# Kernel optimization log

Hardware: AMD Instinct MI355X
Metric: run time of the kernel (lower is better)

The kernel has to match this reference:

```python
import jax, jax.numpy as jnp
import numpy as np

D_IN, D_OUT, RANK, N = 4096, 4096, 16, 8192


def _quantize_weight(w, bits):
    # round-to-nearest fake quantization, stored back as floats (as in the torch code)
    absmax = jnp.abs(w).max()
    scale = (2 ** (bits - 1) - 1) / absmax
    q = jnp.clip(jnp.round(w * scale), -2 ** (bits - 1), 2 ** (bits - 1) - 1)
    return q / scale


def _double_quantization(w, bits):
    absmax = jnp.abs(w).max()
    c1 = (2 ** (bits - 1) - 1) / absmax          # scalar fp32 scale
    q = jnp.clip(jnp.round(w * c1), -2 ** (bits - 1), 2 ** (bits - 1) - 1)
    return c1, q / c1                             # c_kbit_2 has same shape as w


def setup_inputs() -> dict:
    key = jax.random.key(0)
    kX, kW, kL1, kL2 = jax.random.split(key, 4)
    X = jax.random.normal(kX, (N, D_IN), dtype=jnp.float32)
    W0 = jax.random.normal(kW, (D_IN, D_OUT), dtype=jnp.float32)
    W_nf4 = _quantize_weight(W0, bits=4)
    c_fp32_1, c_kbit_2 = _double_quantization(W_nf4, bits=8)
    L1 = jax.random.normal(kL1, (D_IN, RANK), dtype=jnp.float32)
    L2 = jax.random.normal(kL2, (RANK, D_OUT), dtype=jnp.float32)
    return {"X": X, "W_nf4": W_nf4, "c_fp32_1": c_fp32_1,
            "c_kbit_2": c_kbit_2, "L1": L1, "L2": L2}


def reference(X, W_nf4, c_fp32_1, c_kbit_2, L1, L2):
    # dequantize: elementwise scalar * elementwise-tensor scaling of stored weight
    W = W_nf4 * c_fp32_1 * c_kbit_2               # [D_IN, D_OUT]
    # main GEMM + low-rank LoRA path, added in the epilogue
    Y = X @ W + (X @ L1) @ L2                     # [N, D_OUT]
    return Y
```

## Files before the change

### kernel.cpp

```cpp
#include <hip/hip_runtime.h>


#define M_ROWS 8192
#define K_DIM  4096
#define N_OUT  4096
#define CVT_BLOCKS 16384
#define WP_BLOCKS  8192
#define TR_BLOCKS  32

typedef float  f32x16 __attribute__((ext_vector_type(16)));
typedef __bf16 bf16x8 __attribute__((ext_vector_type(8)));
typedef float  f32x4  __attribute__((ext_vector_type(4)));
typedef unsigned short ushort8v __attribute__((ext_vector_type(8)));

__device__ float          Tg[(size_t)M_ROWS * 16];
__device__ unsigned short L1t[16 * K_DIM];
__device__ unsigned short L2t[N_OUT * 16];

__device__ __forceinline__ unsigned short f2bf(float f) {
    __bf16 h = (__bf16)f;
    union { __bf16 h; unsigned short u; } v; v.h = h;
    return v.u;
}

__global__ __launch_bounds__(256) void prep_kernel(
        const float* __restrict__ X,    ushort8v* __restrict__ Xh,
        const float* __restrict__ Wnf4, const float* __restrict__ c1p,
        const float* __restrict__ c2,   const float* __restrict__ L1,
        const float* __restrict__ L2,   unsigned short* __restrict__ Wt) {
    const int t = threadIdx.x;

    if (blockIdx.x < CVT_BLOCKS) {
        size_t tid = (size_t)blockIdx.x * 256 + t;
        const float4* xp = (const float4*)X;
        float4 a = xp[tid * 2];
        float4 b = xp[tid * 2 + 1];
        ushort8v o;
        o[0] = f2bf(a.x); o[1] = f2bf(a.y); o[2] = f2bf(a.z); o[3] = f2bf(a.w);
        o[4] = f2bf(b.x); o[5] = f2bf(b.y); o[6] = f2bf(b.z); o[7] = f2bf(b.w);
        Xh[tid] = o;
        return;
    }

    if (blockIdx.x < CVT_BLOCKS + WP_BLOCKS) {
        const int wb = blockIdx.x - CVT_BLOCKS;
        const int n  = (wb & 63) * 64 + (t & 63);
        const int k0 = (wb >> 6) * 32 + (t >> 6) * 8;
        const float c1 = *c1p;
        ushort8v o;
        #pragma unroll
        for (int kk = 0; kk < 8; ++kk) {
            size_t g = (size_t)(k0 + kk) * N_OUT + n;
            o[kk] = f2bf(Wnf4[g] * c1 * c2[g]);
        }
        *(ushort8v*)&Wt[(size_t)n * K_DIM + k0] = o;
        return;
    }

    const int idx = (blockIdx.x - CVT_BLOCKS - WP_BLOCKS) * 256 + t;
    if (idx < K_DIM) {
        const float4* lp = (const float4*)&L1[(size_t)idx * 16];
        float4 r0 = lp[0], r1 = lp[1], r2 = lp[2], r3 = lp[3];
        float v[16] = {r0.x, r0.y, r0.z, r0.w, r1.x, r1.y, r1.z, r1.w,
                       r2.x, r2.y, r2.z, r2.w, r3.x, r3.y, r3.z, r3.w};
        #pragma unroll
        for (int r = 0; r < 16; ++r)
            L1t[(size_t)r * K_DIM + idx] = f2bf(v[r]);
    } else {
        const int n = idx - K_DIM;
        ushort8v a, b;
        #pragma unroll
        for (int r = 0; r < 8; ++r) a[r] = f2bf(L2[(size_t)r * N_OUT + n]);
        #pragma unroll
        for (int r = 0; r < 8; ++r) b[r] = f2bf(L2[(size_t)(r + 8) * N_OUT + n]);
        *(ushort8v*)&L2t[(size_t)n * 16]     = a;
        *(ushort8v*)&L2t[(size_t)n * 16 + 8] = b;
    }
}

__global__ __launch_bounds__(64) void xl1_kernel(const __bf16* __restrict__ Xh) {
    const int m0   = blockIdx.x * 16;
    const int lane = threadIdx.x;
    const int l15  = lane & 15;
    const int l4   = lane >> 4;

    const __bf16* ap = Xh + (size_t)(m0 + l15) * K_DIM + l4 * 8;
    const __bf16* bp = (const __bf16*)L1t + (size_t)l15 * K_DIM + l4 * 8;

    f32x4 acc = {};
    #pragma unroll 8
    for (int k = 0; k < K_DIM; k += 32) {
        bf16x8 af = *(const bf16x8*)(ap + k);
        bf16x8 bf = *(const bf16x8*)(bp + k);
        acc = __builtin_amdgcn_mfma_f32_16x16x32_bf16(af, bf, acc, 0, 0, 0);
    }
    #pragma unroll
    for (int reg = 0; reg < 4; ++reg)
        Tg[(size_t)(m0 + l4 * 4 + reg) * 16 + l15] = acc[reg];
}

__global__ __launch_bounds__(256) void gemm_bt_kernel(
        const __bf16* __restrict__ A, const __bf16* __restrict__ Bt,
        float* __restrict__ C) {
    __shared__ __bf16 As[128 * 32];
    __shared__ __bf16 Bs[128 * 32];

    const int t    = threadIdx.x;
    const int w    = t >> 6;
    const int lane = t & 63;
    const int half = lane >> 5;
    const int l32  = lane & 31;
    const int m0   = blockIdx.y * 128;
    const int n0   = blockIdx.x * 128;
    const int wm   = (w >> 1) * 64;
    const int wn   = (w & 1) * 64;

    const int srow = lane >> 2;
    const int scol = ((lane & 3) ^ ((lane >> 3) & 3)) * 8;
    const int rsw = (l32 >> 1) & 3;

    f32x16 acc[2][2] = {};

    for (int kb = 0; kb < K_DIM; kb += 32) {
        __syncthreads();
        #pragma unroll
        for (int j = 0; j < 2; ++j) {
            int row = w * 32 + j * 16 + srow;
            const __bf16* gp = A + (size_t)(m0 + row) * K_DIM + kb + scol;
            __builtin_amdgcn_global_load_lds(
                (const __attribute__((address_space(1))) unsigned int*)gp,
                (__attribute__((address_space(3))) unsigned int*)(As + (w * 32 + j * 16) * 32),
                16, 0, 0);
        }
        #pragma unroll
        for (int j = 0; j < 2; ++j) {
            int row = w * 32 + j * 16 + srow;
            const __bf16* gp = Bt + (size_t)(n0 + row) * K_DIM + kb + scol;
            __builtin_amdgcn_global_load_lds(
                (const __attribute__((address_space(1))) unsigned int*)gp,
                (__attribute__((address_space(3))) unsigned int*)(Bs + (w * 32 + j * 16) * 32),
                16, 0, 0);
        }
        __syncthreads();

        bf16x8 af[2][2], bf[2][2];
        #pragma unroll
        for (int mt = 0; mt < 2; ++mt)
            #pragma unroll
            for (int ks = 0; ks < 2; ++ks) {
                int row = wm + mt * 32 + l32;
                int slot = (2 * ks + half) ^ rsw;
                af[mt][ks] = *(const bf16x8*)(As + row * 32 + slot * 8);
            }
        #pragma unroll
        for (int nt = 0; nt < 2; ++nt)
            #pragma unroll
            for (int ks = 0; ks < 2; ++ks) {
                int row = wn + nt * 32 + l32;
                int slot = (2 * ks + half) ^ rsw;
                bf[nt][ks] = *(const bf16x8*)(Bs + row * 32 + slot * 8);
            }

        #pragma unroll
        for (int ks = 0; ks < 2; ++ks)
            #pragma unroll
            for (int mt = 0; mt < 2; ++mt)
                #pragma unroll
                for (int nt = 0; nt < 2; ++nt)
                    acc[mt][nt] = __builtin_amdgcn_mfma_f32_32x32x16_bf16(
                        af[mt][ks], bf[nt][ks], acc[mt][nt], 0, 0, 0);
    }

    {
        bf16x8 afl[2], bfl[2];
        #pragma unroll
        for (int mt = 0; mt < 2; ++mt) {
            const float* tp = Tg + (size_t)(m0 + wm + mt * 32 + l32) * 16 + half * 8;
            float4 p0 = *(const float4*)tp;
            float4 p1 = *(const float4*)(tp + 4);
            afl[mt][0] = (__bf16)p0.x; afl[mt][1] = (__bf16)p0.y;
            afl[mt][2] = (__bf16)p0.z; afl[mt][3] = (__bf16)p0.w;
            afl[mt][4] = (__bf16)p1.x; afl[mt][5] = (__bf16)p1.y;
            afl[mt][6] = (__bf16)p1.z; afl[mt][7] = (__bf16)p1.w;
        }
        #pragma unroll
        for (int nt = 0; nt < 2; ++nt)
            bfl[nt] = *(const bf16x8*)((const __bf16*)L2t +
                        (size_t)(n0 + wn + nt * 32 + l32) * 16 + half * 8);
        #pragma unroll
        for (int mt = 0; mt < 2; ++mt)
            #pragma unroll
            for (int nt = 0; nt < 2; ++nt)
                acc[mt][nt] = __builtin_amdgcn_mfma_f32_32x32x16_bf16(
                    afl[mt], bfl[nt], acc[mt][nt], 0, 0, 0);
    }

    #pragma unroll
    for (int mt = 0; mt < 2; ++mt)
        #pragma unroll
        for (int nt = 0; nt < 2; ++nt) {
            int col = n0 + wn + nt * 32 + l32;
            #pragma unroll
            for (int reg = 0; reg < 16; ++reg) {
                int row = m0 + wm + mt * 32 + (reg & 3) + 8 * (reg >> 2) + 4 * half;
                C[(size_t)row * N_OUT + col] = acc[mt][nt][reg];
            }
        }
}

extern "C" void kernel_launch(void* const* d_in, const int* in_sizes, int n_in,
                              void* d_out, int out_size, void* d_ws, size_t ws_size,
                              hipStream_t stream) {
    const float* X    = (const float*)d_in[0];
    const float* Wnf4 = (const float*)d_in[1];
    const float* c1   = (const float*)d_in[2];
    const float* c2   = (const float*)d_in[3];
    const float* L1   = (const float*)d_in[4];
    const float* L2   = (const float*)d_in[5];
    float* Y = (float*)d_out;

    unsigned short* Xh = (unsigned short*)d_ws;
    unsigned short* Wt = (unsigned short*)((char*)d_ws + (size_t)M_ROWS * K_DIM * 2);

    prep_kernel<<<CVT_BLOCKS + WP_BLOCKS + TR_BLOCKS, 256, 0, stream>>>(
        X, (ushort8v*)Xh, Wnf4, c1, c2, L1, L2, Wt);
    xl1_kernel<<<M_ROWS / 16, 64, 0, stream>>>((const __bf16*)Xh);
    gemm_bt_kernel<<<dim3(N_OUT / 128, M_ROWS / 128), 256, 0, stream>>>(
        (const __bf16*)Xh, (const __bf16*)Wt, Y);
}
```

Before: 649.3 us.

## Split prep kernels, LDS-transpose weights, split-K xl1, swizzle and deepen GEMM K-step

Splits the fused prep kernel into separate conversion, weight-prep and LoRA-prep kernels. Weight prep now reads coalesced float4 rows and transposes them through an LDS tile before writing bf16. The X@L1 kernel spreads K across four waves and reduces the partial sums in shared memory to get more parallelism. The main GEMM remaps block indices so neighbouring blocks share tiles in L2, and it loads two 32-wide K slabs per barrier pair to halve synchronisation. The trade-offs are more kernel launches and twice the LDS per GEMM block.

Result: slower. 663.0 us (+2.1%).

```diff
diff --git a/kernel.cpp b/kernel.cpp
--- a/kernel.cpp
+++ b/kernel.cpp
@@ -5,12 +5,11 @@
 #define K_DIM  4096
 #define N_OUT  4096
 #define CVT_BLOCKS 16384
-#define WP_BLOCKS  8192
-#define TR_BLOCKS  32
+#define WP_BLOCKS  4096
 
 typedef float  f32x16 __attribute__((ext_vector_type(16)));
+typedef float  f32x4  __attribute__((ext_vector_type(4)));
 typedef __bf16 bf16x8 __attribute__((ext_vector_type(8)));
-typedef float  f32x4  __attribute__((ext_vector_type(4)));
 typedef unsigned short ushort8v __attribute__((ext_vector_type(8)));
 
 __device__ float          Tg[(size_t)M_ROWS * 16];
@@ -23,41 +22,54 @@
     return v.u;
 }
 
-__global__ __launch_bounds__(256) void prep_kernel(
-        const float* __restrict__ X,    ushort8v* __restrict__ Xh,
+__global__ __launch_bounds__(256) void cvt_kernel(
+        const float* __restrict__ X, ushort8v* __restrict__ Xh) {
+    size_t tid = (size_t)blockIdx.x * 256 + threadIdx.x;
+    const float4* xp = (const float4*)X;
+    float4 a = xp[tid * 2];
+    float4 b = xp[tid * 2 + 1];
+    ushort8v o;
+    o[0] = f2bf(a.x); o[1] = f2bf(a.y); o[2] = f2bf(a.z); o[3] = f2bf(a.w);
+    o[4] = f2bf(b.x); o[5] = f2bf(b.y); o[6] = f2bf(b.z); o[7] = f2bf(b.w);
+    Xh[tid] = o;
+}
+
+__global__ __launch_bounds__(256) void wprep_kernel(
         const float* __restrict__ Wnf4, const float* __restrict__ c1p,
-        const float* __restrict__ c2,   const float* __restrict__ L1,
-        const float* __restrict__ L2,   unsigned short* __restrict__ Wt) {
-    const int t = threadIdx.x;
-
-    if (blockIdx.x < CVT_BLOCKS) {
-        size_t tid = (size_t)blockIdx.x * 256 + t;
-        const float4* xp = (const float4*)X;
-        float4 a = xp[tid * 2];
-        float4 b = xp[tid * 2 + 1];
-        ushort8v o;
-        o[0] = f2bf(a.x); o[1] = f2bf(a.y); o[2] = f2bf(a.z); o[3] = f2bf(a.w);
-        o[4] = f2bf(b.x); o[5] = f2bf(b.y); o[6] = f2bf(b.z); o[7] = f2bf(b.w);
-        Xh[tid] = o;
-        return;
-    }
-
-    if (blockIdx.x < CVT_BLOCKS + WP_BLOCKS) {
-        const int wb = blockIdx.x - CVT_BLOCKS;
-        const int n  = (wb & 63) * 64 + (t & 63);
-        const int k0 = (wb >> 6) * 32 + (t >> 6) * 8;
-        const float c1 = *c1p;
-        ushort8v o;
-        #pragma unroll
-        for (int kk = 0; kk < 8; ++kk) {
-            size_t g = (size_t)(k0 + kk) * N_OUT + n;
-            o[kk] = f2bf(Wnf4[g] * c1 * c2[g]);
-        }
-        *(ushort8v*)&Wt[(size_t)n * K_DIM + k0] = o;
-        return;
-    }
-
-    const int idx = (blockIdx.x - CVT_BLOCKS - WP_BLOCKS) * 256 + t;
+        const float* __restrict__ c2,   unsigned short* __restrict__ Wt) {
+    __shared__ unsigned short tile[64][72];
+    const int t  = threadIdx.x;
+    const int wb = blockIdx.x;
+    const int n0 = (wb & 63) * 64;
+    const int k0 = (wb >> 6) * 64;
+    const float c1 = *c1p;
+
+    #pragma unroll
+    for (int i = 0; i < 4; ++i) {
+        int idx = i * 1024 + t * 4;
+        int k = idx >> 6, n4 = idx & 63;
+        size_t g = (size_t)(k0 + k) * N_OUT + n0 + n4;
+        float4 w = *(const float4*)&Wnf4[g];
+        float4 s = *(const float4*)&c2[g];
+        tile[n4    ][k] = f2bf(w.x * c1 * s.x);
+        tile[n4 + 1][k] = f2bf(w.y * c1 * s.y);
+        tile[n4 + 2][k] = f2bf(w.z * c1 * s.z);
+        tile[n4 + 3][k] = f2bf(w.w * c1 * s.w);
+    }
+    __syncthreads();
+
+    #pragma unroll
+    for (int i = 0; i < 2; ++i) {
+        int task = i * 256 + t;
+        int n = task >> 3, k8 = (task & 7) * 8;
+        ushort8v o = *(const ushort8v*)&tile[n][k8];
+        *(ushort8v*)&Wt[(size_t)(n0 + n) * K_DIM + k0 + k8] = o;
+    }
+}
+
+__global__ __launch_bounds__(256) void lorap_kernel(
+        const float* __restrict__ L1, const float* __restrict__ L2) {
+    const int idx = blockIdx.x * 256 + threadIdx.x;
     if (idx < K_DIM) {
         const float4* lp = (const float4*)&L1[(size_t)idx * 16];
         float4 r0 = lp[0], r1 = lp[1], r2 = lp[2], r3 = lp[3];
@@ -78,40 +90,71 @@
     }
 }
 
-__global__ __launch_bounds__(64) void xl1_kernel(const __bf16* __restrict__ Xh) {
-    const int m0   = blockIdx.x * 16;
-    const int lane = threadIdx.x;
-    const int l15  = lane & 15;
-    const int l4   = lane >> 4;
-
-    const __bf16* ap = Xh + (size_t)(m0 + l15) * K_DIM + l4 * 8;
-    const __bf16* bp = (const __bf16*)L1t + (size_t)l15 * K_DIM + l4 * 8;
-
+__global__ __launch_bounds__(256) void xl1_kernel(const __bf16* __restrict__ Xh) {
+    __shared__ float red[4][256];
+    const int m0 = blockIdx.x * 16;
+    const int t = threadIdx.x, wv = t >> 6, lane = t & 63;
+    const int l15 = lane & 15, l4 = lane >> 4;
+    const __bf16* ap = Xh + (size_t)(m0 + l15) * K_DIM + wv * 1024 + l4 * 8;
+    const __bf16* bp = (const __bf16*)L1t + (size_t)l15 * K_DIM + wv * 1024 + l4 * 8;
     f32x4 acc = {};
     #pragma unroll 8
-    for (int k = 0; k < K_DIM; k += 32) {
-        bf16x8 af = *(const bf16x8*)(ap + k);
-        bf16x8 bf = *(const bf16x8*)(bp + k);
-        acc = __builtin_amdgcn_mfma_f32_16x16x32_bf16(af, bf, acc, 0, 0, 0);
-    }
-    #pragma unroll
-    for (int reg = 0; reg < 4; ++reg)
-        Tg[(size_t)(m0 + l4 * 4 + reg) * 16 + l15] = acc[reg];
-}
+    for (int k = 0; k < 1024; k += 32) {
+        bf16x8 a = *(const bf16x8*)(ap + k);
+        bf16x8 b = *(const bf16x8*)(bp + k);
+        acc = __builtin_amdgcn_mfma_f32_16x16x32_bf16(a, b, acc, 0, 0, 0);
+    }
+    #pragma unroll
+    for (int r = 0; r < 4; ++r) red[wv][(l4 * 4 + r) * 16 + l15] = acc[r];
+    __syncthreads();
+    if (wv == 0) {
+        #pragma unroll
+        for (int r = 0; r < 4; ++r) {
+            int e = (l4 * 4 + r) * 16 + l15;
+            Tg[(size_t)(m0 + l4 * 4 + r) * 16 + l15] =
+                red[0][e] + red[1][e] + red[2][e] + red[3][e];
+        }
+    }
+}
+
+#define COMPUTE(B) do { \
+    bf16x8 af[2][2], bf[2][2]; \
+    _Pragma("unroll") for (int mt = 0; mt < 2; ++mt) \
+      _Pragma("unroll") for (int ks = 0; ks < 2; ++ks) { \
+        int row = wm + mt * 32 + l32; \
+        int slot = (2 * ks + half) ^ rsw; \
+        af[mt][ks] = *(const bf16x8*)(&As[B][0] + row * 32 + slot * 8); \
+      } \
+    _Pragma("unroll") for (int nt = 0; nt < 2; ++nt) \
+      _Pragma("unroll") for (int ks = 0; ks < 2; ++ks) { \
+        int row = wn + nt * 32 + l32; \
+        int slot = (2 * ks + half) ^ rsw; \
+        bf[nt][ks] = *(const bf16x8*)(&Bs[B][0] + row * 32 + slot * 8); \
+      } \
+    _Pragma("unroll") for (int ks = 0; ks < 2; ++ks) \
+      _Pragma("unroll") for (int mt = 0; mt < 2; ++mt) \
+        _Pragma("unroll") for (int nt = 0; nt < 2; ++nt) \
+          acc[mt][nt] = __builtin_amdgcn_mfma_f32_32x32x16_bf16( \
+              af[mt][ks], bf[nt][ks], acc[mt][nt], 0, 0, 0); \
+} while (0)
 
 __global__ __launch_bounds__(256) void gemm_bt_kernel(
         const __bf16* __restrict__ A, const __bf16* __restrict__ Bt,
         float* __restrict__ C) {
-    __shared__ __bf16 As[128 * 32];
-    __shared__ __bf16 Bs[128 * 32];
+    __shared__ __bf16 As[2][128 * 32];
+    __shared__ __bf16 Bs[2][128 * 32];
 
     const int t    = threadIdx.x;
     const int w    = t >> 6;
     const int lane = t & 63;
     const int half = lane >> 5;
     const int l32  = lane & 31;
-    const int m0   = blockIdx.y * 128;
-    const int n0   = blockIdx.x * 128;
+
+    const int bid = blockIdx.x;
+    const int swz = (bid & 7) * 256 + (bid >> 3);
+    const int m0  = (swz >> 5) * 128;
+    const int n0  = (swz & 31) * 128;
+
     const int wm   = (w >> 1) * 64;
     const int wn   = (w & 1) * 64;
 
@@ -121,54 +164,35 @@
 
     f32x16 acc[2][2] = {};
 
-    for (int kb = 0; kb < K_DIM; kb += 32) {
+    for (int kb = 0; kb < K_DIM; kb += 64) {
         __syncthreads();
         #pragma unroll
-        for (int j = 0; j < 2; ++j) {
-            int row = w * 32 + j * 16 + srow;
-            const __bf16* gp = A + (size_t)(m0 + row) * K_DIM + kb + scol;
-            __builtin_amdgcn_global_load_lds(
-                (const __attribute__((address_space(1))) unsigned int*)gp,
-                (__attribute__((address_space(3))) unsigned int*)(As + (w * 32 + j * 16) * 32),
-                16, 0, 0);
-        }
-        #pragma unroll
-        for (int j = 0; j < 2; ++j) {
-            int row = w * 32 + j * 16 + srow;
-            const __bf16* gp = Bt + (size_t)(n0 + row) * K_DIM + kb + scol;
-            __builtin_amdgcn_global_load_lds(
-                (const __attribute__((address_space(1))) unsigned int*)gp,
-                (__attribute__((address_space(3))) unsigned int*)(Bs + (w * 32 + j * 16) * 32),
-                16, 0, 0);
+        for (int b = 0; b < 2; ++b) {
+            #pragma unroll
+            for (int j = 0; j < 2; ++j) {
+                int row = w * 32 + j * 16 + srow;
+                const __bf16* gp = A + (size_t)(m0 + row) * K_DIM + kb + b * 32 + scol;
+                __builtin_amdgcn_global_load_lds(
+                    (const __attribute__((address_space(1))) unsigned int*)gp,
+                    (__attribute__((address_space(3))) unsigned int*)
+                        (&As[b][0] + (w * 32 + j * 16) * 32),
+                    16, 0, 0);
+            }
+            #pragma unroll
+            for (int j = 0; j < 2; ++j) {
+                int row = w * 32 + j * 16 + srow;
+                const __bf16* gp = Bt + (size_t)(n0 + row) * K_DIM + kb + b * 32 + scol;
+                __builtin_amdgcn_global_load_lds(
+                    (const __attribute__((address_space(1))) unsigned int*)gp,
+                    (__attribute__((address_space(3))) unsigned int*)
+                        (&Bs[b][0] + (w * 32 + j * 16) * 32),
+                    16, 0, 0);
+            }
         }
         __syncthreads();
 
-        bf16x8 af[2][2], bf[2][2];
-        #pragma unroll
-        for (int mt = 0; mt < 2; ++mt)
-            #pragma unroll
-            for (int ks = 0; ks < 2; ++ks) {
-                int row = wm + mt * 32 + l32;
-                int slot = (2 * ks + half) ^ rsw;
-                af[mt][ks] = *(const bf16x8*)(As + row * 32 + slot * 8);
-            }
-        #pragma unroll
-        for (int nt = 0; nt < 2; ++nt)
-            #pragma unroll
-            for (int ks = 0; ks < 2; ++ks) {
-                int row = wn + nt * 32 + l32;
-                int slot = (2 * ks + half) ^ rsw;
-                bf[nt][ks] = *(const bf16x8*)(Bs + row * 32 + slot * 8);
-            }
-
-        #pragma unroll
-        for (int ks = 0; ks < 2; ++ks)
-            #pragma unroll
-            for (int mt = 0; mt < 2; ++mt)
-                #pragma unroll
-                for (int nt = 0; nt < 2; ++nt)
-                    acc[mt][nt] = __builtin_amdgcn_mfma_f32_32x32x16_bf16(
-                        af[mt][ks], bf[nt][ks], acc[mt][nt], 0, 0, 0);
+        COMPUTE(0);
+        COMPUTE(1);
     }
 
     {
@@ -222,9 +246,10 @@
     unsigned short* Xh = (unsigned short*)d_ws;
     unsigned short* Wt = (unsigned short*)((char*)d_ws + (size_t)M_ROWS * K_DIM * 2);
 
-    prep_kernel<<<CVT_BLOCKS + WP_BLOCKS + TR_BLOCKS, 256, 0, stream>>>(
-        X, (ushort8v*)Xh, Wnf4, c1, c2, L1, L2, Wt);
-    xl1_kernel<<<M_ROWS / 16, 64, 0, stream>>>((const __bf16*)Xh);
-    gemm_bt_kernel<<<dim3(N_OUT / 128, M_ROWS / 128), 256, 0, stream>>>(
+    cvt_kernel<<<CVT_BLOCKS, 256, 0, stream>>>(X, (ushort8v*)Xh);
+    wprep_kernel<<<WP_BLOCKS, 256, 0, stream>>>(Wnf4, c1, c2, Wt);
+    lorap_kernel<<<32, 256, 0, stream>>>(L1, L2);
+    xl1_kernel<<<M_ROWS / 16, 256, 0, stream>>>((const __bf16*)Xh);
+    gemm_bt_kernel<<<(M_ROWS / 128) * (N_OUT / 128), 256, 0, stream>>>(
         (const __bf16*)Xh, (const __bf16*)Wt, Y);
 }
```
